# Optimization experiments

Measured on AMD Instinct MI355X. Metric: run time of the kernel, lower is better.

Reference implementation:

```python
import jax, jax.numpy as jnp
import numpy as np

DISTANCE_W = 1.0
ANGLE_W = 1.0
EPS = 1e-12  # matches F.normalize eps


def setup_inputs() -> dict:
    key = jax.random.key(0)
    k1, k2 = jax.random.split(key)
    student_emb = jax.random.normal(k1, (1024, 512), dtype=jnp.float32)
    teacher_emb = jax.random.normal(k2, (1024, 512), dtype=jnp.float32)
    return {"student_emb": student_emb, "teacher_emb": teacher_emb}


def _pairwise_similarity(emb):
    # F.normalize(emb, dim=1) then emb @ emb.T -> [N, N] cosine similarity
    norm = jnp.maximum(jnp.linalg.norm(emb, axis=1, keepdims=True), EPS)
    en = emb / norm
    return en @ en.T


def _angle_similarity(emb):
    # ||e_i - e_j||^2 for all pairs, computed via the GEMM expansion
    # (same math as the N x N x D broadcast in the original, no O(N^2 D) tensor)
    sq = jnp.sum(emb * emb, axis=1)  # [N]
    gram = emb @ emb.T               # [N, N]
    return sq[:, None] + sq[None, :] - 2.0 * gram


def reference(student_emb, teacher_emb):
    loss_dist = jnp.mean((_pairwise_similarity(student_emb) - _pairwise_similarity(teacher_emb)) ** 2)
    loss_angle = jnp.mean((_angle_similarity(student_emb) - _angle_similarity(teacher_emb)) ** 2)
    return DISTANCE_W * loss_dist + ANGLE_W * loss_angle
```

## Files before the change

### kernel.cpp

```cpp
#include <hip/hip_runtime.h>

typedef short short8 __attribute__((ext_vector_type(8)));
typedef float f32x4 __attribute__((ext_vector_type(4)));
typedef unsigned short ushort;

#define DD 512


__device__ __forceinline__ short to_bf16(float f) {
    unsigned int u = __float_as_uint(f);
    u += 0x7FFFu + ((u >> 16) & 1u);
    return (short)(u >> 16);
}

__device__ __forceinline__ short8 pack8(float4 a, float4 b) {
    short8 r;
    r[0] = to_bf16(a.x); r[1] = to_bf16(a.y); r[2] = to_bf16(a.z); r[3] = to_bf16(a.w);
    r[4] = to_bf16(b.x); r[5] = to_bf16(b.y); r[6] = to_bf16(b.z); r[7] = to_bf16(b.w);
    return r;
}

__device__ __forceinline__ float dot4(float4 v) {
    return v.x*v.x + v.y*v.y + v.z*v.z + v.w*v.w;
}

__global__ __launch_bounds__(64) void convert_kernel(const float* __restrict__ S,
                                                     const float* __restrict__ T,
                                                     ushort* __restrict__ bf,
                                                     float* __restrict__ sqarr,
                                                     float* __restrict__ accw) {
    const int idx  = blockIdx.x;
    const int lane = threadIdx.x;
    const float* src = (idx < 1024) ? (S + (size_t)idx * DD)
                                    : (T + (size_t)(idx - 1024) * DD);
    float4 v0 = ((const float4*)src)[lane * 2];
    float4 v1 = ((const float4*)src)[lane * 2 + 1];
    *(short8*)(bf + (size_t)idx * DD + lane * 8) = pack8(v0, v1);
    float s = dot4(v0) + dot4(v1);
    #pragma unroll
    for (int off = 32; off > 0; off >>= 1) s += __shfl_down(s, off);
    if (lane == 0) {
        sqarr[idx]        = s;
        sqarr[2048 + idx] = 1.0f / fmaxf(sqrtf(s), 1e-12f);
        if (idx == 0) { accw[0] = 0.0f; ((unsigned int*)accw)[1] = 0u; }
    }
}

__global__ __launch_bounds__(256, 2) void rkd_tile_kernel(const ushort* __restrict__ bf,
                                                          const float* __restrict__ sqarr,
                                                          float* __restrict__ accw,
                                                          float* __restrict__ out) {
    __shared__ ushort AS[64][64], AT[64][64];
    __shared__ ushort BS[32][64], BT[32][64];
    __shared__ float wsum[4];

    const int t = threadIdx.x;
    const int I = (blockIdx.x >> 5) * 64;
    const int J = (blockIdx.x & 31) * 32;
    const int w = t >> 6;
    const int L = t & 63;
    const int m = L & 15;
    const int quad = L >> 4;
    const int arow = w * 16 + m;

    const ushort* bS = bf;
    const ushort* bT = bf + (size_t)1024 * DD;

    const int lrow = L >> 3;
    const int lchk = (L & 7) ^ lrow;
    const int lgoff = lrow * DD + lchk * 8;

    const ushort* gtab[6];
    ushort* ltab[6];
    #pragma unroll
    for (int j = 0; j < 6; ++j) {
        const int q = w * 6 + j;
        const ushort* gmat; ushort* lmat; int rbase, gbase;
        if (q < 8)       { gmat = bS; lmat = &AS[0][0]; rbase = q * 8;        gbase = I; }
        else if (q < 16) { gmat = bT; lmat = &AT[0][0]; rbase = (q - 8) * 8;  gbase = I; }
        else if (q < 20) { gmat = bS; lmat = &BS[0][0]; rbase = (q - 16) * 8; gbase = J; }
        else             { gmat = bT; lmat = &BT[0][0]; rbase = (q - 20) * 8; gbase = J; }
        gtab[j] = gmat + (size_t)(gbase + rbase) * DD + lgoff;
        ltab[j] = lmat + rbase * 64;
    }

    f32x4 aS0 = {0,0,0,0}, aS1 = {0,0,0,0};
    f32x4 aT0 = {0,0,0,0}, aT1 = {0,0,0,0};

    for (int k0 = 0; k0 < DD; k0 += 64) {
        __syncthreads();
        #pragma unroll
        for (int j = 0; j < 6; ++j)
            __builtin_amdgcn_global_load_lds(
                (const __attribute__((address_space(1))) void*)(gtab[j] + k0),
                (__attribute__((address_space(3))) void*)ltab[j], 16, 0, 0);
        __syncthreads();

        #pragma unroll
        for (int ks = 0; ks < 2; ++ks) {
            const int cs = (((ks * 4 + quad) ^ (m & 7))) * 8;
            short8 af_s = *(const short8*)&AS[arow][cs];
            short8 af_t = *(const short8*)&AT[arow][cs];
            short8 b_s0 = *(const short8*)&BS[m][cs];
            short8 b_s1 = *(const short8*)&BS[16 + m][cs];
            short8 b_t0 = *(const short8*)&BT[m][cs];
            short8 b_t1 = *(const short8*)&BT[16 + m][cs];
            aS0 = __builtin_amdgcn_mfma_f32_16x16x32_bf16(af_s, b_s0, aS0, 0, 0, 0);
            aS1 = __builtin_amdgcn_mfma_f32_16x16x32_bf16(af_s, b_s1, aS1, 0, 0, 0);
            aT0 = __builtin_amdgcn_mfma_f32_16x16x32_bf16(af_t, b_t0, aT0, 0, 0, 0);
            aT1 = __builtin_amdgcn_mfma_f32_16x16x32_bf16(af_t, b_t1, aT1, 0, 0, 0);
        }
    }

    const int j0 = J + m, j1 = J + 16 + m;
    float js0 = sqarr[j0],        jt0 = sqarr[1024 + j0];
    float rjs0 = sqarr[2048 + j0], rjt0 = sqarr[3072 + j0];
    float js1 = sqarr[j1],        jt1 = sqarr[1024 + j1];
    float rjs1 = sqarr[2048 + j1], rjt1 = sqarr[3072 + j1];

    float local = 0.0f;
    const int ib = I + w * 16 + quad * 4;
    #pragma unroll
    for (int reg = 0; reg < 4; ++reg) {
        const int r = ib + reg;
        float is = sqarr[r],        it = sqarr[1024 + r];
        float ris = sqarr[2048 + r], rit = sqarr[3072 + r];

        float gs0 = aS0[reg], gt0 = aT0[reg];
        float d1 = gs0 * ris * rjs0 - gt0 * rit * rjt0;
        float d2 = (is + js0 - 2.0f * gs0) - (it + jt0 - 2.0f * gt0);
        local += d1 * d1 + d2 * d2;

        float gs1 = aS1[reg], gt1 = aT1[reg];
        float e1 = gs1 * ris * rjs1 - gt1 * rit * rjt1;
        float e2 = (is + js1 - 2.0f * gs1) - (it + jt1 - 2.0f * gt1);
        local += e1 * e1 + e2 * e2;
    }

    #pragma unroll
    for (int off = 32; off > 0; off >>= 1) local += __shfl_down(local, off);
    if (L == 0) wsum[w] = local;
    __syncthreads();

    if (t == 0) {
        float blk = wsum[0] + wsum[1] + wsum[2] + wsum[3];
        atomicAdd(&accw[0], blk);
        __threadfence();
        unsigned int old = atomicAdd((unsigned int*)accw + 1, 1u);
        if (old == 511u) {
            float tot = atomicAdd(&accw[0], 0.0f);
            out[0] = tot * (1.0f / 1048576.0f);
        }
    }
}

extern "C" void kernel_launch(void* const* d_in, const int* in_sizes, int n_in,
                              void* d_out, int out_size, void* d_ws, size_t ws_size,
                              hipStream_t stream) {
    const float* S = (const float*)d_in[0];
    const float* T = (const float*)d_in[1];
    ushort* bf   = (ushort*)d_ws;
    float* sqarr = (float*)((char*)d_ws + 2 * 1024 * 1024);
    float* accw  = sqarr + 4096;
    float* out   = (float*)d_out;

    convert_kernel<<<2048, 64, 0, stream>>>(S, T, bf, sqarr, accw);
    rkd_tile_kernel<<<512, 256, 0, stream>>>(bf, sqarr, accw, out);
}
```

Measured before the change: 78.69 us.

## Double-buffer LDS tiles, prefetch sqarr, spread atomics, widen convert blocks

The tile kernel now double-buffers its shared-memory tiles, issuing the async global-to-LDS loads for the next K slice before computing on the current one. This removes one barrier per iteration and overlaps memory with MFMA work. The per-row norm values are loaded before the main loop, and the block sums are spread over 16 atomic slots to cut contention on a single address. The convert kernel handles four rows per 256-thread block. The trade-off is twice the LDS (48KB), which may limit occupancy, plus a slightly more complex final reduction.

```diff
diff --git a/kernel.cpp b/kernel.cpp
--- a/kernel.cpp
+++ b/kernel.cpp
@@ -24,34 +24,34 @@
     return v.x*v.x + v.y*v.y + v.z*v.z + v.w*v.w;
 }
 
-__global__ __launch_bounds__(64) void convert_kernel(const float* __restrict__ S,
-                                                     const float* __restrict__ T,
-                                                     ushort* __restrict__ bf,
-                                                     float* __restrict__ sqarr,
-                                                     float* __restrict__ accw) {
-    const int idx  = blockIdx.x;
-    const int lane = threadIdx.x;
-    const float* src = (idx < 1024) ? (S + (size_t)idx * DD)
-                                    : (T + (size_t)(idx - 1024) * DD);
+__global__ __launch_bounds__(256) void convert_kernel(const float* __restrict__ S,
+                                                      const float* __restrict__ T,
+                                                      ushort* __restrict__ bf,
+                                                      float* __restrict__ sqarr,
+                                                      float* __restrict__ accw) {
+    const int t    = threadIdx.x;
+    const int lane = t & 63;
+    const int row  = blockIdx.x * 4 + (t >> 6);
+    const float* src = (row < 1024) ? (S + (size_t)row * DD)
+                                    : (T + (size_t)(row - 1024) * DD);
     float4 v0 = ((const float4*)src)[lane * 2];
     float4 v1 = ((const float4*)src)[lane * 2 + 1];
-    *(short8*)(bf + (size_t)idx * DD + lane * 8) = pack8(v0, v1);
+    *(short8*)(bf + (size_t)row * DD + lane * 8) = pack8(v0, v1);
     float s = dot4(v0) + dot4(v1);
     #pragma unroll
     for (int off = 32; off > 0; off >>= 1) s += __shfl_down(s, off);
     if (lane == 0) {
-        sqarr[idx]        = s;
-        sqarr[2048 + idx] = 1.0f / fmaxf(sqrtf(s), 1e-12f);
-        if (idx == 0) { accw[0] = 0.0f; ((unsigned int*)accw)[1] = 0u; }
+        sqarr[row]        = s;
+        sqarr[2048 + row] = 1.0f / fmaxf(sqrtf(s), 1e-12f);
     }
+    if (blockIdx.x == 0 && t < 17) ((unsigned int*)(accw))[t] = 0u;
 }
 
 __global__ __launch_bounds__(256, 2) void rkd_tile_kernel(const ushort* __restrict__ bf,
                                                           const float* __restrict__ sqarr,
                                                           float* __restrict__ accw,
                                                           float* __restrict__ out) {
-    __shared__ ushort AS[64][64], AT[64][64];
-    __shared__ ushort BS[32][64], BT[32][64];
+    __shared__ ushort tiles[2][12288];
     __shared__ float wsum[4];
 
     const int t = threadIdx.x;
@@ -66,45 +66,70 @@
     const ushort* bS = bf;
     const ushort* bT = bf + (size_t)1024 * DD;
 
-    const int lrow = L >> 3;
-    const int lchk = (L & 7) ^ lrow;
+    const int lrow  = L >> 3;
+    const int lchk  = (L & 7) ^ lrow;
     const int lgoff = lrow * DD + lchk * 8;
 
     const ushort* gtab[6];
-    ushort* ltab[6];
+    int loff[6];
     #pragma unroll
     for (int j = 0; j < 6; ++j) {
         const int q = w * 6 + j;
-        const ushort* gmat; ushort* lmat; int rbase, gbase;
-        if (q < 8)       { gmat = bS; lmat = &AS[0][0]; rbase = q * 8;        gbase = I; }
-        else if (q < 16) { gmat = bT; lmat = &AT[0][0]; rbase = (q - 8) * 8;  gbase = I; }
-        else if (q < 20) { gmat = bS; lmat = &BS[0][0]; rbase = (q - 16) * 8; gbase = J; }
-        else             { gmat = bT; lmat = &BT[0][0]; rbase = (q - 20) * 8; gbase = J; }
-        gtab[j] = gmat + (size_t)(gbase + rbase) * DD + lgoff;
-        ltab[j] = lmat + rbase * 64;
+        const ushort* gmat; int gbase, lo;
+        if (q < 8)       { gmat = bS; gbase = I; lo = 0     + q * 512; }
+        else if (q < 16) { gmat = bT; gbase = I; lo = 4096  + (q - 8) * 512; }
+        else if (q < 20) { gmat = bS; gbase = J; lo = 8192  + (q - 16) * 512; }
+        else             { gmat = bT; gbase = J; lo = 10240 + (q - 20) * 512; }
+        const int rbase = (lo & 4095) >> 6;
+        (void)rbase;
+        gtab[j] = gmat + (size_t)gbase * DD + (size_t)((lo * 8) & 0)  + lgoff
+                  + (size_t)(((q < 8) ? q : (q < 16) ? (q - 8) : (q < 20) ? (q - 16) : (q - 20)) * 8) * DD;
+        loff[j] = lo;
+    }
+
+    const int j0 = J + m, j1 = J + 16 + m;
+    const float js0 = sqarr[j0],        jt0 = sqarr[1024 + j0];
+    const float rjs0 = sqarr[2048 + j0], rjt0 = sqarr[3072 + j0];
+    const float js1 = sqarr[j1],        jt1 = sqarr[1024 + j1];
+    const float rjs1 = sqarr[2048 + j1], rjt1 = sqarr[3072 + j1];
+    const int ib = I + w * 16 + quad * 4;
+    float isv[4], itv[4], risv[4], ritv[4];
+    #pragma unroll
+    for (int reg = 0; reg < 4; ++reg) {
+        isv[reg]  = sqarr[ib + reg];        itv[reg]  = sqarr[1024 + ib + reg];
+        risv[reg] = sqarr[2048 + ib + reg]; ritv[reg] = sqarr[3072 + ib + reg];
     }
 
     f32x4 aS0 = {0,0,0,0}, aS1 = {0,0,0,0};
     f32x4 aT0 = {0,0,0,0}, aT1 = {0,0,0,0};
 
-    for (int k0 = 0; k0 < DD; k0 += 64) {
+    #pragma unroll
+    for (int j = 0; j < 6; ++j)
+        __builtin_amdgcn_global_load_lds(
+            (const __attribute__((address_space(1))) void*)(gtab[j]),
+            (__attribute__((address_space(3))) void*)(&tiles[0][0] + loff[j]), 16, 0, 0);
+
+    for (int i = 0; i < 8; ++i) {
         __syncthreads();
-        #pragma unroll
-        for (int j = 0; j < 6; ++j)
-            __builtin_amdgcn_global_load_lds(
-                (const __attribute__((address_space(1))) void*)(gtab[j] + k0),
-                (__attribute__((address_space(3))) void*)ltab[j], 16, 0, 0);
-        __syncthreads();
-
+        if (i < 7) {
+            const int nb = (i + 1) & 1;
+            const int k0 = (i + 1) * 64;
+            #pragma unroll
+            for (int j = 0; j < 6; ++j)
+                __builtin_amdgcn_global_load_lds(
+                    (const __attribute__((address_space(1))) void*)(gtab[j] + k0),
+                    (__attribute__((address_space(3))) void*)(&tiles[nb][0] + loff[j]), 16, 0, 0);
+        }
+        const ushort* base = &tiles[i & 1][0];
         #pragma unroll
         for (int ks = 0; ks < 2; ++ks) {
-            const int cs = (((ks * 4 + quad) ^ (m & 7))) * 8;
-            short8 af_s = *(const short8*)&AS[arow][cs];
-            short8 af_t = *(const short8*)&AT[arow][cs];
-            short8 b_s0 = *(const short8*)&BS[m][cs];
-            short8 b_s1 = *(const short8*)&BS[16 + m][cs];
-            short8 b_t0 = *(const short8*)&BT[m][cs];
-            short8 b_t1 = *(const short8*)&BT[16 + m][cs];
+            const int cs = ((ks * 4 + quad) ^ (m & 7)) * 8;
+            short8 af_s = *(const short8*)(base + arow * 64 + cs);
+            short8 af_t = *(const short8*)(base + 4096 + arow * 64 + cs);
+            short8 b_s0 = *(const short8*)(base + 8192 + m * 64 + cs);
+            short8 b_s1 = *(const short8*)(base + 8192 + (16 + m) * 64 + cs);
+            short8 b_t0 = *(const short8*)(base + 10240 + m * 64 + cs);
+            short8 b_t1 = *(const short8*)(base + 10240 + (16 + m) * 64 + cs);
             aS0 = __builtin_amdgcn_mfma_f32_16x16x32_bf16(af_s, b_s0, aS0, 0, 0, 0);
             aS1 = __builtin_amdgcn_mfma_f32_16x16x32_bf16(af_s, b_s1, aS1, 0, 0, 0);
             aT0 = __builtin_amdgcn_mfma_f32_16x16x32_bf16(af_t, b_t0, aT0, 0, 0, 0);
@@ -112,19 +137,10 @@
         }
     }
 
-    const int j0 = J + m, j1 = J + 16 + m;
-    float js0 = sqarr[j0],        jt0 = sqarr[1024 + j0];
-    float rjs0 = sqarr[2048 + j0], rjt0 = sqarr[3072 + j0];
-    float js1 = sqarr[j1],        jt1 = sqarr[1024 + j1];
-    float rjs1 = sqarr[2048 + j1], rjt1 = sqarr[3072 + j1];
-
     float local = 0.0f;
-    const int ib = I + w * 16 + quad * 4;
     #pragma unroll
     for (int reg = 0; reg < 4; ++reg) {
-        const int r = ib + reg;
-        float is = sqarr[r],        it = sqarr[1024 + r];
-        float ris = sqarr[2048 + r], rit = sqarr[3072 + r];
+        float is = isv[reg], it = itv[reg], ris = risv[reg], rit = ritv[reg];
 
         float gs0 = aS0[reg], gt0 = aT0[reg];
         float d1 = gs0 * ris * rjs0 - gt0 * rit * rjt0;
@@ -144,11 +160,15 @@
 
     if (t == 0) {
         float blk = wsum[0] + wsum[1] + wsum[2] + wsum[3];
-        atomicAdd(&accw[0], blk);
+        atomicAdd(&accw[blockIdx.x & 15], blk);
         __threadfence();
-        unsigned int old = atomicAdd((unsigned int*)accw + 1, 1u);
+        unsigned int old = atomicAdd((unsigned int*)(accw + 16), 1u);
         if (old == 511u) {
-            float tot = atomicAdd(&accw[0], 0.0f);
+            __threadfence();
+            float tot = 0.0f;
+            #pragma unroll
+            for (int s2 = 0; s2 < 16; ++s2)
+                tot += __hip_atomic_load(&accw[s2], __ATOMIC_RELAXED, __HIP_MEMORY_SCOPE_AGENT);
             out[0] = tot * (1.0f / 1048576.0f);
         }
     }
@@ -164,6 +184,6 @@
     float* accw  = sqarr + 4096;
     float* out   = (float*)d_out;
 
-    convert_kernel<<<2048, 64, 0, stream>>>(S, T, bf, sqarr, accw);
+    convert_kernel<<<512, 256, 0, stream>>>(S, T, bf, sqarr, accw);
     rkd_tile_kernel<<<512, 256, 0, stream>>>(bf, sqarr, accw, out);
 }
```

New measurement: 75.93 us. -3.5%, faster.
